# Kernel tuning notes

Measured on AMD Instinct MI355X. Metric: run time of the kernel, lower is better.

Reference implementation:

```python
import jax, jax.numpy as jnp
import numpy as np

B, C, O, H, W = 8, 64, 64, 128, 128


def conv3x3(x, w, b):
    # x: [B,Cin,H,W], w: [Cout,Cin,3,3], stride 1, padding 1
    y = jax.lax.conv_general_dilated(
        x, w, window_strides=(1, 1), padding=((1, 1), (1, 1)),
        dimension_numbers=("NCHW", "OIHW", "NCHW"))
    return y + b[None, :, None, None]


def setup_inputs() -> dict:
    key = jax.random.key(0)
    ks = jax.random.split(key, 6)
    fan = C * 9
    x = jax.random.normal(ks[0], (B, C, H, W), dtype=jnp.float32)
    w_main = jax.random.normal(ks[1], (O, C, 3, 3), dtype=jnp.float32) / np.sqrt(fan)
    # small offset weights keep sampled locations near the regular grid (realistic post-training regime)
    w_offset = jax.random.normal(ks[2], (18, C, 3, 3), dtype=jnp.float32) * 0.05 / np.sqrt(fan)
    b_offset = jnp.zeros((18,), dtype=jnp.float32)
    w_mask = jax.random.normal(ks[3], (9, C, 3, 3), dtype=jnp.float32) / np.sqrt(fan)
    b_mask = jnp.zeros((9,), dtype=jnp.float32)
    return {"x": x, "w_main": w_main, "w_offset": w_offset,
            "b_offset": b_offset, "w_mask": w_mask, "b_mask": b_mask}


def deform_conv2d(x, w_main, offset, mask):
    # torchvision.ops.deform_conv2d: kernel 3x3, stride 1, pad 1, dilation 1, no bias
    Bb, Cc, Hh, Ww = x.shape
    Oo = w_main.shape[0]
    off = offset.reshape(Bb, 9, 2, Hh, Ww)
    dy, dx = off[:, :, 0], off[:, :, 1]            # [B,9,H,W]; pairs ordered (y,x), k row-major
    k = jnp.arange(9)
    kh = (k // 3 - 1).astype(x.dtype)              # kernel row offset in {-1,0,1}
    kw = (k % 3 - 1).astype(x.dtype)
    iy = jnp.arange(Hh, dtype=x.dtype)
    ix = jnp.arange(Ww, dtype=x.dtype)
    # sampling positions p = p0 + p_k + delta_p
    py = dy + iy[None, None, :, None] + kh[None, :, None, None]
    px = dx + ix[None, None, None, :] + kw[None, :, None, None]

    y0 = jnp.floor(py)
    x0 = jnp.floor(px)
    ly = py - y0
    lx = px - x0
    y0i = y0.astype(jnp.int32)
    x0i = x0.astype(jnp.int32)
    y1i = y0i + 1
    x1i = x0i + 1

    bidx = jnp.arange(Bb)[:, None, None, None]

    def corner(yi, xi, wgt):
        # zero-padding semantics: out-of-bounds neighbors contribute 0
        valid = (yi >= 0) & (yi < Hh) & (xi >= 0) & (xi < Ww)
        v = x[bidx, :, jnp.clip(yi, 0, Hh - 1), jnp.clip(xi, 0, Ww - 1)]  # [B,9,H,W,C]
        return v * (wgt * valid)[..., None]

    samp = (corner(y0i, x0i, (1 - ly) * (1 - lx))
            + corner(y0i, x1i, (1 - ly) * lx)
            + corner(y1i, x0i, ly * (1 - lx))
            + corner(y1i, x1i, ly * lx))
    samp = samp * mask[..., None]                  # modulation mask (dcn v2)
    # contract sampled patches with weights: [B,9,H,W,C] x [O,C,9] -> [B,O,H,W]
    return jnp.einsum("bkhwc,ock->bohw", samp, w_main.reshape(Oo, Cc, 9))


def reference(x, w_main, w_offset, b_offset, w_mask, b_mask):
    offset = conv3x3(x, w_offset, b_offset)                 # [B,18,H,W]
    mask = jax.nn.sigmoid(conv3x3(x, w_mask, b_mask))       # [B,9,H,W]
    return deform_conv2d(x, w_main, offset, mask)
```

## Files before the change

### kernel.cpp

```cpp
#include <hip/hip_runtime.h>
#include <math.h>

#define BB 8
#define CC 64
#define OO 64
#define HH 128
#define WW 128
#define HW (HH*WW)
#define NPIX (BB*HW)

typedef __bf16 bf16x8 __attribute__((ext_vector_type(8)));
typedef float floatx4 __attribute__((ext_vector_type(4)));
typedef float f32x2  __attribute__((ext_vector_type(2)));
typedef unsigned short ushort_t;

#define XT_BYTES  16777216
#define WT_BYTES  73728

__device__ __forceinline__ unsigned short f2b(float f) {
    unsigned u = __float_as_uint(f);
    u += 0x7fffu + ((u >> 16) & 1u);
    return (unsigned short)(u >> 16);
}

__global__ __launch_bounds__(256) void transpose_kernel(
    const float* __restrict__ x, ushort_t* __restrict__ xt)
{
    __shared__ float tile[64][33];
    int bh = blockIdx.x;
    int w0 = blockIdx.y * 32;
    int b  = bh >> 7;
    int h  = bh & 127;
    int t  = threadIdx.x;
    int tx = t & 31;
    int ty = t >> 5;

    #pragma unroll
    for (int j = 0; j < 8; ++j) {
        int c = ty * 8 + j;
        tile[c][tx] = x[(((size_t)(b*CC + c))*HH + h)*WW + (w0 + tx)];
    }
    __syncthreads();
    #pragma unroll
    for (int j = 0; j < 4; ++j) {
        int w  = ty + 8*j;
        int cp = tx;
        unsigned u = (unsigned)f2b(tile[2*cp][w]) |
                     ((unsigned)f2b(tile[2*cp+1][w]) << 16);
        *(unsigned*)(xt + (((size_t)(b*HH + h))*WW + (w0 + w))*CC + 2*cp) = u;
    }
}

__global__ __launch_bounds__(256) void repack_kernel(
    const float* __restrict__ wm, const float* __restrict__ woff,
    const float* __restrict__ wmask, ushort_t* __restrict__ wt,
    ushort_t* __restrict__ wb)
{
    int i = blockIdx.x * 256 + threadIdx.x;
    if (i < 36864) {
        int o = i / 576, k = i % 576, tap = k >> 6, c = k & 63;
        wt[i] = f2b(wm[o*576 + c*9 + tap]);
    }
    int j = i - 36864;
    if (j >= 0 && j < 18432) {
        int o = j / 576, k = j % 576, tap = k >> 6, c = k & 63;
        float v = 0.f;
        if (o < 18)      v = woff[o*576 + c*9 + tap];
        else if (o < 27) v = wmask[(o-18)*576 + c*9 + tap];
        wb[j] = f2b(v);
    }
}

#define WR 14
#define WSTRIDE 72

__global__ __launch_bounds__(256) void fused_kernel(
    const ushort_t* __restrict__ xt, const ushort_t* __restrict__ wb,
    const float* __restrict__ boff, const float* __restrict__ bmsk,
    const ushort_t* __restrict__ wt, float* __restrict__ out)
{
    __shared__ ushort_t win[WR*WR*WSTRIDE];
    __shared__ ushort_t samp[2*64*72];
    __shared__ float    om_lds[64*28];

    int t = threadIdx.x;
    int lane = t & 63, wv = t >> 6;
    int bid = blockIdx.x;
    int b  = bid >> 8;
    int th = (bid >> 4) & 15;
    int tw = bid & 15;
    int h0 = th * 8, w0 = tw * 8;
    const ushort_t* xbase = xt + ((size_t)b << 20);

    for (int idx = t; idx < WR*WR*8; idx += 256) {
        int r   = idx / (WR*8);
        int rem = idx - r*(WR*8);
        int col = rem >> 3;
        int ch  = (rem & 7) << 3;
        int y = h0 + r - 3, x = w0 + col - 3;
        uint4 val = make_uint4(0,0,0,0);
        if ((unsigned)y < (unsigned)HH && (unsigned)x < (unsigned)WW)
            val = *(const uint4*)(xbase + (((y << 7) + x) << 6) + ch);
        *(uint4*)(win + (r*WR + col)*WSTRIDE + ch) = val;
    }
    __syncthreads();

    int n = lane & 15, quad = lane >> 4;

    {
        const ushort_t* wb0 = wb + n*576;
        const ushort_t* wb1 = wb + (16 + n)*576;
        floatx4 acc0 = {0.f,0.f,0.f,0.f}, acc1 = {0.f,0.f,0.f,0.f};
        int trow = wv*2 + (n >> 3);
        int tcol = n & 7;

        #pragma unroll
        for (int s = 0; s < 18; ++s) {
            int tap  = s >> 1;
            int tr   = tap / 3, tc = tap % 3;
            int coff = (s & 1)*32 + quad*8;
            int kk = tap*64 + coff;
            bf16x8 b0 = *(const bf16x8*)(wb0 + kk);
            bf16x8 b1 = *(const bf16x8*)(wb1 + kk);
            bf16x8 a = *(const bf16x8*)(win +
                ((trow + tr + 2)*WR + (tcol + tc + 2))*WSTRIDE + coff);
            acc0 = __builtin_amdgcn_mfma_f32_16x16x32_bf16(a, b0, acc0, 0, 0, 0);
            acc1 = __builtin_amdgcn_mfma_f32_16x16x32_bf16(a, b1, acc1, 0, 0, 0);
        }

        #pragma unroll
        for (int r = 0; r < 4; ++r) {
            int p = wv*16 + quad*4 + r;
            float* dst = om_lds + p*28;
            dst[n] = acc0[r] + boff[n];
            int o1 = 16 + n;
            if (o1 < 18) {
                dst[o1] = acc1[r] + boff[o1];
            } else if (o1 < 27) {
                float z = acc1[r] + bmsk[o1 - 18];
                dst[o1] = 1.f / (1.f + expf(-z));
            }
        }
    }
    __syncthreads();

    int pa = t >> 2, cg = t & 3;
    int ph = pa >> 3, pw = pa & 7;
    int h_a = h0 + ph, w_a = w0 + pw;
    const float* omp = om_lds + pa*28;

    floatx4 acc[4];
    #pragma unroll
    for (int i = 0; i < 4; ++i) acc[i] = (floatx4){0.f,0.f,0.f,0.f};
    const ushort_t* wrow = wt + (wv*16 + n)*576;

    for (int k = 0; k < 9; ++k) {
        ushort_t* sb = samp + (k & 1) * (64*72);

        int kr = k / 3, kc = k - kr*3;
        float dy = omp[2*k], dx = omp[2*k + 1], m = omp[18 + k];
        float py = (float)(h_a + kr - 1) + dy;
        float px = (float)(w_a + kc - 1) + dx;
        float y0f = floorf(py), x0f = floorf(px);
        float ly = py - y0f, lx = px - x0f;
        int y0 = (int)y0f, x0 = (int)x0f, y1 = y0 + 1, x1 = x0 + 1;
        float vy0 = ((unsigned)y0 < (unsigned)HH) ? 1.f : 0.f;
        float vy1 = ((unsigned)y1 < (unsigned)HH) ? 1.f : 0.f;
        float vx0 = ((unsigned)x0 < (unsigned)WW) ? 1.f : 0.f;
        float vx1 = ((unsigned)x1 < (unsigned)WW) ? 1.f : 0.f;

        float cw[4] = { (1.f-ly)*(1.f-lx)*vy0*vx0*m,
                        (1.f-ly)*lx      *vy0*vx1*m,
                        ly*(1.f-lx)      *vy1*vx0*m,
                        ly*lx            *vy1*vx1*m };
        int ys[4] = { y0, y0, y1, y1 };
        int xs[4] = { x0, x1, x0, x1 };

        f32x2 v2[8];
        #pragma unroll
        for (int i = 0; i < 8; ++i) v2[i] = (f32x2){0.f, 0.f};

        #pragma unroll
        for (int cn = 0; cn < 4; ++cn) {
            int yc = min(max(ys[cn], 0), HH-1);
            int xc = min(max(xs[cn], 0), WW-1);
            int wy = yc - h0 + 3, wx = xc - w0 + 3;
            uint4 q0, q1;
            if ((unsigned)wy < (unsigned)WR && (unsigned)wx < (unsigned)WR) {
                const uint4* cp = (const uint4*)(win + (wy*WR + wx)*WSTRIDE + cg*16);
                q0 = cp[0]; q1 = cp[1];
            } else {
                const uint4* cp = (const uint4*)(xbase + (((yc << 7) + xc) << 6) + cg*16);
                q0 = cp[0]; q1 = cp[1];
            }
            unsigned d[8] = { q0.x, q0.y, q0.z, q0.w, q1.x, q1.y, q1.z, q1.w };
            float wg = cw[cn];
            #pragma unroll
            for (int j = 0; j < 8; ++j) {
                f32x2 e;
                e.x = __uint_as_float(d[j] << 16);
                e.y = __uint_as_float(d[j] & 0xffff0000u);
                v2[j] += e * wg;
            }
        }

        {
            unsigned uu[8];
            #pragma unroll
            for (int j = 0; j < 8; ++j)
                uu[j] = (unsigned)f2b(v2[j].x) | ((unsigned)f2b(v2[j].y) << 16);
            uint4* dst = (uint4*)(sb + pa*72 + cg*16);
            dst[0] = make_uint4(uu[0], uu[1], uu[2], uu[3]);
            dst[1] = make_uint4(uu[4], uu[5], uu[6], uu[7]);
        }
        __syncthreads();

        #pragma unroll
        for (int half = 0; half < 2; ++half) {
            bf16x8 bfrag = *(const bf16x8*)(wrow + k*64 + half*32 + quad*8);
            #pragma unroll
            for (int mt = 0; mt < 4; ++mt) {
                bf16x8 afrag = *(const bf16x8*)(sb + (mt*16 + n)*72 + half*32 + quad*8);
                acc[mt] = __builtin_amdgcn_mfma_f32_16x16x32_bf16(afrag, bfrag, acc[mt], 0, 0, 0);
            }
        }
        __syncthreads();
    }

    float* op = out + ((size_t)b*OO + (wv*16 + n))*HW;
    #pragma unroll
    for (int mt = 0; mt < 4; ++mt) {
        int row = h0 + mt*2 + (quad >> 1);
        int col = w0 + (quad & 1)*4;
        float4 st = make_float4(acc[mt][0], acc[mt][1], acc[mt][2], acc[mt][3]);
        *(float4*)(op + row*WW + col) = st;
    }
}

extern "C" void kernel_launch(void* const* d_in, const int* in_sizes, int n_in,
                              void* d_out, int out_size, void* d_ws, size_t ws_size,
                              hipStream_t stream)
{
    const float* x      = (const float*)d_in[0];
    const float* w_main = (const float*)d_in[1];
    const float* w_off  = (const float*)d_in[2];
    const float* b_off  = (const float*)d_in[3];
    const float* w_msk  = (const float*)d_in[4];
    const float* b_msk  = (const float*)d_in[5];
    float* out = (float*)d_out;

    unsigned char* ws = (unsigned char*)d_ws;
    ushort_t* xt = (ushort_t*)ws;
    ushort_t* wt = (ushort_t*)(ws + XT_BYTES);
    ushort_t* wb = (ushort_t*)(ws + XT_BYTES + WT_BYTES);

    dim3 tgrid(BB*HH, WW/32);
    transpose_kernel<<<tgrid, 256, 0, stream>>>(x, xt);

    repack_kernel<<<(36864 + 18432 + 255)/256, 256, 0, stream>>>(
        w_main, w_off, w_msk, wt, wb);

    fused_kernel<<<NPIX/64, 256, 0, stream>>>(xt, wb, b_off, b_msk, wt, out);
}
```

Baseline: 190.9 us.

## Widen transpose tiles, shrink halo window, single-buffer samples with software-pipelined gather

The transpose kernel now processes a full 128-wide row per block using float4 loads and 16-byte bf16 stores, cutting the number of blocks and narrow memory transactions. In the fused kernel the LDS halo window drops from 14x14 to 12x12 and the offset/mask LDS stride becomes 29 to avoid bank conflicts. The bilinear gather for tap k+1 is issued after the MFMAs of tap k, so it can overlap them, and the sample buffer is single-buffered to save LDS and raise occupancy. The smaller window sends more off-grid samples to the global-memory fallback, and the one-tap-ahead gather holds more registers live.

Result: faster. 171.2 us (-10.3%).

```diff
diff --git a/kernel.cpp b/kernel.cpp
--- a/kernel.cpp
+++ b/kernel.cpp
@@ -26,28 +26,34 @@
 __global__ __launch_bounds__(256) void transpose_kernel(
     const float* __restrict__ x, ushort_t* __restrict__ xt)
 {
-    __shared__ float tile[64][33];
+    __shared__ float tile[64*129];
     int bh = blockIdx.x;
-    int w0 = blockIdx.y * 32;
-    int b  = bh >> 7;
-    int h  = bh & 127;
-    int t  = threadIdx.x;
-    int tx = t & 31;
-    int ty = t >> 5;
-
-    #pragma unroll
-    for (int j = 0; j < 8; ++j) {
-        int c = ty * 8 + j;
-        tile[c][tx] = x[(((size_t)(b*CC + c))*HH + h)*WW + (w0 + tx)];
+    int b = bh >> 7, h = bh & 127;
+    int t = threadIdx.x;
+
+    const float* xrow = x + ((size_t)b*CC*HH + h)*WW;
+    #pragma unroll
+    for (int it = 0; it < 8; ++it) {
+        int c = it*8 + (t >> 5);
+        int w = (t & 31) * 4;
+        float4 v = *(const float4*)(xrow + (size_t)c*HW + w);
+        float* dst = tile + c*129 + w;
+        dst[0] = v.x; dst[1] = v.y; dst[2] = v.z; dst[3] = v.w;
     }
     __syncthreads();
-    #pragma unroll
-    for (int j = 0; j < 4; ++j) {
-        int w  = ty + 8*j;
-        int cp = tx;
-        unsigned u = (unsigned)f2b(tile[2*cp][w]) |
-                     ((unsigned)f2b(tile[2*cp+1][w]) << 16);
-        *(unsigned*)(xt + (((size_t)(b*HH + h))*WW + (w0 + w))*CC + 2*cp) = u;
+    ushort_t* orow = xt + (((size_t)(b*HH + h))*WW) * CC;
+    #pragma unroll
+    for (int it = 0; it < 4; ++it) {
+        int w  = it*32 + (t >> 3);
+        int cg = t & 7;
+        unsigned uu[4];
+        #pragma unroll
+        for (int j = 0; j < 4; ++j) {
+            float lo = tile[(cg*8 + 2*j)*129 + w];
+            float hi = tile[(cg*8 + 2*j + 1)*129 + w];
+            uu[j] = (unsigned)f2b(lo) | ((unsigned)f2b(hi) << 16);
+        }
+        *(uint4*)(orow + (size_t)w*CC + cg*8) = make_uint4(uu[0],uu[1],uu[2],uu[3]);
     }
 }
 
@@ -71,8 +77,9 @@
     }
 }
 
-#define WR 14
+#define WR 12
 #define WSTRIDE 72
+#define OMS 29
 
 __global__ __launch_bounds__(256) void fused_kernel(
     const ushort_t* __restrict__ xt, const ushort_t* __restrict__ wb,
@@ -80,8 +87,8 @@
     const ushort_t* __restrict__ wt, float* __restrict__ out)
 {
     __shared__ ushort_t win[WR*WR*WSTRIDE];
-    __shared__ ushort_t samp[2*64*72];
-    __shared__ float    om_lds[64*28];
+    __shared__ ushort_t samp[64*72];
+    __shared__ float    om_lds[64*OMS];
 
     int t = threadIdx.x;
     int lane = t & 63, wv = t >> 6;
@@ -97,7 +104,7 @@
         int rem = idx - r*(WR*8);
         int col = rem >> 3;
         int ch  = (rem & 7) << 3;
-        int y = h0 + r - 3, x = w0 + col - 3;
+        int y = h0 + r - 2, x = w0 + col - 2;
         uint4 val = make_uint4(0,0,0,0);
         if ((unsigned)y < (unsigned)HH && (unsigned)x < (unsigned)WW)
             val = *(const uint4*)(xbase + (((y << 7) + x) << 6) + ch);
@@ -123,7 +130,7 @@
             bf16x8 b0 = *(const bf16x8*)(wb0 + kk);
             bf16x8 b1 = *(const bf16x8*)(wb1 + kk);
             bf16x8 a = *(const bf16x8*)(win +
-                ((trow + tr + 2)*WR + (tcol + tc + 2))*WSTRIDE + coff);
+                ((trow + tr + 1)*WR + (tcol + tc + 1))*WSTRIDE + coff);
             acc0 = __builtin_amdgcn_mfma_f32_16x16x32_bf16(a, b0, acc0, 0, 0, 0);
             acc1 = __builtin_amdgcn_mfma_f32_16x16x32_bf16(a, b1, acc1, 0, 0, 0);
         }
@@ -131,7 +138,7 @@
         #pragma unroll
         for (int r = 0; r < 4; ++r) {
             int p = wv*16 + quad*4 + r;
-            float* dst = om_lds + p*28;
+            float* dst = om_lds + p*OMS;
             dst[n] = acc0[r] + boff[n];
             int o1 = 16 + n;
             if (o1 < 18) {
@@ -147,16 +154,14 @@
     int pa = t >> 2, cg = t & 3;
     int ph = pa >> 3, pw = pa & 7;
     int h_a = h0 + ph, w_a = w0 + pw;
-    const float* omp = om_lds + pa*28;
+    const float* omp = om_lds + pa*OMS;
 
     floatx4 acc[4];
     #pragma unroll
     for (int i = 0; i < 4; ++i) acc[i] = (floatx4){0.f,0.f,0.f,0.f};
     const ushort_t* wrow = wt + (wv*16 + n)*576;
 
-    for (int k = 0; k < 9; ++k) {
-        ushort_t* sb = samp + (k & 1) * (64*72);
-
+    auto computeA = [&](int k, f32x2* v2) {
         int kr = k / 3, kc = k - kr*3;
         float dy = omp[2*k], dx = omp[2*k + 1], m = omp[18 + k];
         float py = (float)(h_a + kr - 1) + dy;
@@ -176,7 +181,6 @@
         int ys[4] = { y0, y0, y1, y1 };
         int xs[4] = { x0, x1, x0, x1 };
 
-        f32x2 v2[8];
         #pragma unroll
         for (int i = 0; i < 8; ++i) v2[i] = (f32x2){0.f, 0.f};
 
@@ -184,7 +188,7 @@
         for (int cn = 0; cn < 4; ++cn) {
             int yc = min(max(ys[cn], 0), HH-1);
             int xc = min(max(xs[cn], 0), WW-1);
-            int wy = yc - h0 + 3, wx = xc - w0 + 3;
+            int wy = yc - h0 + 2, wx = xc - w0 + 2;
             uint4 q0, q1;
             if ((unsigned)wy < (unsigned)WR && (unsigned)wx < (unsigned)WR) {
                 const uint4* cp = (const uint4*)(win + (wy*WR + wx)*WSTRIDE + cg*16);
@@ -203,13 +207,18 @@
                 v2[j] += e * wg;
             }
         }
-
+    };
+
+    f32x2 v2[8];
+    computeA(0, v2);
+
+    for (int k = 0; k < 9; ++k) {
         {
             unsigned uu[8];
             #pragma unroll
             for (int j = 0; j < 8; ++j)
                 uu[j] = (unsigned)f2b(v2[j].x) | ((unsigned)f2b(v2[j].y) << 16);
-            uint4* dst = (uint4*)(sb + pa*72 + cg*16);
+            uint4* dst = (uint4*)(samp + pa*72 + cg*16);
             dst[0] = make_uint4(uu[0], uu[1], uu[2], uu[3]);
             dst[1] = make_uint4(uu[4], uu[5], uu[6], uu[7]);
         }
@@ -220,10 +229,12 @@
             bf16x8 bfrag = *(const bf16x8*)(wrow + k*64 + half*32 + quad*8);
             #pragma unroll
             for (int mt = 0; mt < 4; ++mt) {
-                bf16x8 afrag = *(const bf16x8*)(sb + (mt*16 + n)*72 + half*32 + quad*8);
+                bf16x8 afrag = *(const bf16x8*)(samp + (mt*16 + n)*72 + half*32 + quad*8);
                 acc[mt] = __builtin_amdgcn_mfma_f32_16x16x32_bf16(afrag, bfrag, acc[mt], 0, 0, 0);
             }
         }
+        if (k < 8) computeA(k + 1, v2);
+
         __syncthreads();
     }
 
@@ -254,8 +265,7 @@
     ushort_t* wt = (ushort_t*)(ws + XT_BYTES);
     ushort_t* wb = (ushort_t*)(ws + XT_BYTES + WT_BYTES);
 
-    dim3 tgrid(BB*HH, WW/32);
-    transpose_kernel<<<tgrid, 256, 0, stream>>>(x, xt);
+    transpose_kernel<<<BB*HH, 256, 0, stream>>>(x, xt);
 
     repack_kernel<<<(36864 + 18432 + 255)/256, 256, 0, stream>>>(
         w_main, w_off, w_msk, wt, wb);
```
